# Kernel optimization log

Measured on AMD Instinct MI355X. Metric: run time of the kernel, lower is better.

Reference implementation:

```python
import jax, jax.numpy as jnp
import numpy as np

DIM = 2048
DIM_HEAD = 128
HEADS = 16
FF_MULT = 4
ATTN_INNER = DIM_HEAD * HEADS            # 2048
FF_INNER = DIM * FF_MULT                 # 8192
FUSED_OUT = ATTN_INNER + 2 * DIM_HEAD + 2 * FF_INNER  # 18688
EPS = 1e-5


def setup_inputs() -> dict:
    key = jax.random.key(0)
    ks = jax.random.split(key, 5)
    B, N = 1, 2048
    x = jax.random.normal(ks[0], (B, N, DIM), dtype=jnp.float32)
    gamma = jnp.ones((DIM,), dtype=jnp.float32)
    # store weights as [in, out] for x @ W
    w_fused = jax.random.normal(ks[1], (DIM, FUSED_OUT), dtype=jnp.float32) * (DIM ** -0.5)
    w_attn_out = jax.random.normal(ks[2], (ATTN_INNER, DIM), dtype=jnp.float32) * (ATTN_INNER ** -0.5)
    w_ff_out = jax.random.normal(ks[3], (FF_INNER, DIM), dtype=jnp.float32) * (FF_INNER ** -0.5)
    return {"x": x, "gamma": gamma, "w_fused": w_fused,
            "w_attn_out": w_attn_out, "w_ff_out": w_ff_out}


def reference(x, gamma, w_fused, w_attn_out, w_ff_out):
    b, n, d = x.shape
    h, dh = HEADS, DIM_HEAD
    scale = dh ** -0.5

    # LayerNorm (beta fixed at 0)
    mu = jnp.mean(x, axis=-1, keepdims=True)
    var = jnp.mean(jnp.square(x - mu), axis=-1, keepdims=True)
    xn = (x - mu) * jax.lax.rsqrt(var + EPS) * gamma

    # fused QKV + FF projection
    proj = xn @ w_fused  # [b, n, FUSED_OUT]
    q = proj[..., :ATTN_INNER]
    k = proj[..., ATTN_INNER:ATTN_INNER + dh]
    v = proj[..., ATTN_INNER + dh:ATTN_INNER + 2 * dh]
    ff = proj[..., ATTN_INNER + 2 * dh:]

    # multi-query attention: q per-head, k/v shared
    q = q.reshape(b, n, h, dh).transpose(0, 2, 1, 3) * scale  # [b,h,n,dh]
    sim = jnp.einsum('bhid,bjd->bhij', q, k)
    causal = jnp.triu(jnp.ones((n, n), dtype=bool), k=1)
    neg = -jnp.finfo(sim.dtype).max
    sim = jnp.where(causal, neg, sim)
    attn = jax.nn.softmax(sim, axis=-1)
    out = jnp.einsum('bhij,bjd->bhid', attn, v)
    out = out.transpose(0, 2, 1, 3).reshape(b, n, h * dh)
    attn_out = out @ w_attn_out

    # parallel SwiGLU FFN
    ff_x, gate = jnp.split(ff, 2, axis=-1)
    ff_out = (jax.nn.silu(gate) * ff_x) @ w_ff_out

    return attn_out + ff_out
```

## Files before the change

kernel.cpp:

```cpp
#include <hip/hip_runtime.h>
#include <hip/hip_bf16.h>

typedef unsigned short u16;
typedef __bf16 bf16x8 __attribute__((ext_vector_type(8)));
typedef float f32x4 __attribute__((ext_vector_type(4)));

#define DIM 2048
#define SEQ 2048
#define HEADS 16
#define DH 128
#define FUSED_OUT 18688
#define FF_INNER 8192
#define KOFF 2048
#define VOFF 2176
#define FFOFF 2304
#define AE_LD 10240

#define WS_XN   0
#define WS_WFT  8388608
#define WS_PROJ 84934656
#define WS_VT   161480704
#define WS_BTE  0
#define WS_AE   41943040

__device__ __forceinline__ float b2f(u16 u) {
  union { unsigned int i; float f; } c; c.i = ((unsigned int)u) << 16; return c.f;
}
__device__ __forceinline__ u16 f2b(float f) {
  union { float f; unsigned int i; } c; c.f = f;
  return (u16)((c.i + 0x7fffu + ((c.i >> 16) & 1u)) >> 16);
}
__device__ __forceinline__ void async16(void* lds, const void* g) {
  __builtin_amdgcn_global_load_lds((const __attribute__((address_space(1))) unsigned int*)g,
                                   (__attribute__((address_space(3))) unsigned int*)lds,
                                   16, 0, 0);
}

union U8 { uint4 v; u16 s[8]; };

__global__ void __launch_bounds__(256) ln_kernel(const float* __restrict__ x,
                                                 const float* __restrict__ gamma,
                                                 u16* __restrict__ xn) {
  const int row = blockIdx.x, tid = threadIdx.x;
  const int lane = tid & 63, wv = tid >> 6;
  float v[8], s1 = 0.f, s2 = 0.f;
  {
    float4 a0 = *(const float4*)(x + (size_t)row * DIM + tid * 8);
    float4 a1 = *(const float4*)(x + (size_t)row * DIM + tid * 8 + 4);
    v[0] = a0.x; v[1] = a0.y; v[2] = a0.z; v[3] = a0.w;
    v[4] = a1.x; v[5] = a1.y; v[6] = a1.z; v[7] = a1.w;
  }
#pragma unroll
  for (int i = 0; i < 8; ++i) { s1 += v[i]; s2 += v[i] * v[i]; }
#pragma unroll
  for (int off = 32; off > 0; off >>= 1) {
    s1 += __shfl_down(s1, off, 64);
    s2 += __shfl_down(s2, off, 64);
  }
  __shared__ float r1[4], r2[4];
  if (lane == 0) { r1[wv] = s1; r2[wv] = s2; }
  __syncthreads();
  s1 = r1[0] + r1[1] + r1[2] + r1[3];
  s2 = r2[0] + r2[1] + r2[2] + r2[3];
  const float inv = 1.0f / DIM;
  const float mu = s1 * inv;
  const float var = s2 * inv - mu * mu;
  const float rs = rsqrtf(var + 1e-5f);
  float4 g0 = *(const float4*)(gamma + tid * 8);
  float4 g1 = *(const float4*)(gamma + tid * 8 + 4);
  const float gm[8] = {g0.x, g0.y, g0.z, g0.w, g1.x, g1.y, g1.z, g1.w};
  U8 o;
#pragma unroll
  for (int i = 0; i < 8; ++i) o.s[i] = f2b((v[i] - mu) * rs * gm[i]);
  *(uint4*)(xn + (size_t)row * DIM + tid * 8) = o.v;
}

__global__ void __launch_bounds__(256) transpose_f2b64(const float* __restrict__ in,
                                                       u16* __restrict__ out,
                                                       int ldin, int ldout) {
  __shared__ u16 t[64][65];
  const int tx = threadIdx.x, ty = threadIdx.y;
  const int r0 = blockIdx.y * 64, c0 = blockIdx.x * 64;
#pragma unroll
  for (int i = 0; i < 16; ++i)
    t[ty + i * 4][tx] = f2b(in[(size_t)(r0 + ty + i * 4) * ldin + c0 + tx]);
  __syncthreads();
#pragma unroll
  for (int i = 0; i < 16; ++i)
    out[(size_t)(c0 + ty + i * 4) * ldout + r0 + tx] = t[tx][ty + i * 4];
}

__global__ void __launch_bounds__(256) trans_wout64(const float* __restrict__ w_attn,
                                                    const float* __restrict__ w_ff,
                                                    u16* __restrict__ BtE) {
  __shared__ u16 t[64][65];
  const int tx = threadIdx.x, ty = threadIdx.y;
  const int c0 = blockIdx.x * 64;
  const float* in; int r0, kout;
  if (blockIdx.y < 32) { in = w_attn; r0 = blockIdx.y * 64; kout = r0; }
  else { in = w_ff; r0 = (blockIdx.y - 32) * 64; kout = 2048 + r0; }
#pragma unroll
  for (int i = 0; i < 16; ++i)
    t[ty + i * 4][tx] = f2b(in[(size_t)(r0 + ty + i * 4) * DIM + c0 + tx]);
  __syncthreads();
#pragma unroll
  for (int i = 0; i < 16; ++i)
    BtE[(size_t)(c0 + ty + i * 4) * AE_LD + kout + tx] = t[tx][ty + i * 4];
}

__global__ void __launch_bounds__(256) transpose_u16_64(const u16* __restrict__ in,
                                                        u16* __restrict__ out,
                                                        int ldin, int ldout) {
  __shared__ u16 t[64][65];
  const int tx = threadIdx.x, ty = threadIdx.y;
  const int r0 = blockIdx.y * 64, c0 = blockIdx.x * 64;
#pragma unroll
  for (int i = 0; i < 16; ++i)
    t[ty + i * 4][tx] = in[(size_t)(r0 + ty + i * 4) * ldin + c0 + tx];
  __syncthreads();
#pragma unroll
  for (int i = 0; i < 16; ++i)
    out[(size_t)(c0 + ty + i * 4) * ldout + r0 + tx] = t[tx][ty + i * 4];
}

template <int OUTMODE>
__global__ void __launch_bounds__(256) gemm_bt(const u16* __restrict__ A,
                                               const u16* __restrict__ Bt,
                                               void* __restrict__ Cv,
                                               int Ksz, int lda, int ldb, int ldc) {
  __shared__ alignas(16) u16 sA[128 * 64];
  __shared__ alignas(16) u16 sB[128 * 64];
  const int tid = threadIdx.x;
  const int lane = tid & 63, wv = tid >> 6;
  const int lhalf = lane & 15, lgrp = lane >> 4;
  const int m0 = blockIdx.x * 128, n0 = blockIdx.y * 128;
  const int kbeg = blockIdx.z * Ksz, kend = kbeg + Ksz;
  const int wr = (wv >> 1) * 64, wc = (wv & 1) * 64;
  const f32x4 fzero = {0.f, 0.f, 0.f, 0.f};

  const int srow = lane >> 3;
  const int scol = ((lane & 7) ^ srow) * 8;
  const int key = lhalf & 7;

  f32x4 acc[4][4];
#pragma unroll
  for (int i = 0; i < 4; ++i)
#pragma unroll
    for (int j = 0; j < 4; ++j) acc[i][j] = fzero;

  for (int k0 = kbeg; k0 < kend; k0 += 64) {
#pragma unroll
    for (int c = 0; c < 4; ++c) {
      const int row = c * 32 + wv * 8 + srow;
      const int ldsoff = (c * 4096 + wv * 1024) >> 1;
      async16(&sA[ldsoff], A + (size_t)(m0 + row) * lda + k0 + scol);
      async16(&sB[ldsoff], Bt + (size_t)(n0 + row) * ldb + k0 + scol);
    }
    __syncthreads();
#pragma unroll
    for (int kk = 0; kk < 64; kk += 32) {
      bf16x8 af[4], bfr[4];
#pragma unroll
      for (int i = 0; i < 4; ++i)
        af[i] = *(const bf16x8*)&sA[(wr + i * 16 + lhalf) * 64 + ((((kk >> 3) + lgrp) ^ key) << 3)];
#pragma unroll
      for (int j = 0; j < 4; ++j)
        bfr[j] = *(const bf16x8*)&sB[(wc + j * 16 + lhalf) * 64 + ((((kk >> 3) + lgrp) ^ key) << 3)];
#pragma unroll
      for (int i = 0; i < 4; ++i)
#pragma unroll
        for (int j = 0; j < 4; ++j)
          acc[i][j] = __builtin_amdgcn_mfma_f32_16x16x32_bf16(af[i], bfr[j], acc[i][j], 0, 0, 0);
    }
    __syncthreads();
  }
#pragma unroll
  for (int i = 0; i < 4; ++i)
#pragma unroll
    for (int j = 0; j < 4; ++j)
#pragma unroll
      for (int t = 0; t < 4; ++t) {
        const int row = m0 + wr + i * 16 + lgrp * 4 + t;
        const int col = n0 + wc + j * 16 + lhalf;
        if (OUTMODE == 0) ((u16*)Cv)[(size_t)row * ldc + col] = f2b(acc[i][j][t]);
        else atomicAdd((float*)Cv + (size_t)row * ldc + col, acc[i][j][t]);
      }
}

__global__ void __launch_bounds__(256) attn_kernel(const u16* __restrict__ proj,
                                                   const u16* __restrict__ Vt,
                                                   u16* __restrict__ Ae) {
  const int h = blockIdx.y, qi = blockIdx.x;
  const int tid = threadIdx.x;
  const int lane = tid & 63, wv = tid >> 6;
  const int lhalf = lane & 15, lgrp = lane >> 4;
  const int key = lhalf & 7;

  __shared__ alignas(16) u16 Ks[128 * 128];
  __shared__ alignas(16) u16 Vts[128 * 128];
  __shared__ alignas(16) u16 Ps[4][16 * 128];

  const int sr = lane >> 4;
  const int sb = lane & 15;

  bf16x8 aq[4];
  {
    const u16* gq = proj + (size_t)(qi * 64 + wv * 16 + lhalf) * FUSED_OUT + h * DH;
#pragma unroll
    for (int kk = 0; kk < 4; ++kk) aq[kk] = *(const bf16x8*)(gq + kk * 32 + lgrp * 8);
  }
  const f32x4 fzero = {0.f, 0.f, 0.f, 0.f};
  f32x4 o[8];
#pragma unroll
  for (int i = 0; i < 8; ++i) o[i] = fzero;
  float mrow[4] = {-__builtin_inff(), -__builtin_inff(), -__builtin_inff(), -__builtin_inff()};
  float lrow[4] = {0.f, 0.f, 0.f, 0.f};
  const float scale = 0.088388347648318447f;
  const int jmax = (qi * 64 + 63) >> 7;

  for (int jt = 0; jt <= jmax; ++jt) {
    __syncthreads();
#pragma unroll
    for (int i = 0; i < 8; ++i) {
      const int ch = wv * 8 + i;
      const int row = ch * 4 + sr;
      const int gb = sb ^ (row & 7);
      async16(&Ks[ch * 512], proj + (size_t)(jt * 128 + row) * FUSED_OUT + KOFF + gb * 8);
      async16(&Vts[ch * 512], Vt + (size_t)row * SEQ + jt * 128 + gb * 8);
    }
    __syncthreads();
    f32x4 s[8];
#pragma unroll
    for (int sub = 0; sub < 8; ++sub) {
      f32x4 a = fzero;
#pragma unroll
      for (int kk = 0; kk < 4; ++kk) {
        bf16x8 bk = *(const bf16x8*)&Ks[(sub * 16 + lhalf) * 128 + (((kk * 4 + lgrp) ^ key) << 3)];
        a = __builtin_amdgcn_mfma_f32_16x16x32_bf16(aq[kk], bk, a, 0, 0, 0);
      }
      s[sub] = a;
    }
    const int row_g = qi * 64 + wv * 16 + lgrp * 4;
    const int col_b = jt * 128 + lhalf;
#pragma unroll
    for (int t = 0; t < 4; ++t) {
      float mx = -__builtin_inff();
#pragma unroll
      for (int sub = 0; sub < 8; ++sub) {
        float v = s[sub][t] * scale;
        if (col_b + sub * 16 > row_g + t) v = -__builtin_inff();
        s[sub][t] = v;
        mx = fmaxf(mx, v);
      }
      mx = fmaxf(mx, __shfl_xor(mx, 1, 64));
      mx = fmaxf(mx, __shfl_xor(mx, 2, 64));
      mx = fmaxf(mx, __shfl_xor(mx, 4, 64));
      mx = fmaxf(mx, __shfl_xor(mx, 8, 64));
      const float mnew = fmaxf(mrow[t], mx);
      const float alpha = __expf(mrow[t] - mnew);
      mrow[t] = mnew;
      float ls = 0.f;
#pragma unroll
      for (int sub = 0; sub < 8; ++sub) {
        const float p = __expf(s[sub][t] - mnew);
        s[sub][t] = p;
        ls += p;
      }
      ls += __shfl_xor(ls, 1, 64);
      ls += __shfl_xor(ls, 2, 64);
      ls += __shfl_xor(ls, 4, 64);
      ls += __shfl_xor(ls, 8, 64);
      lrow[t] = lrow[t] * alpha + ls;
      const int prow = lgrp * 4 + t;
      const int pkey = prow & 7;
#pragma unroll
      for (int sub = 0; sub < 8; ++sub) {
        o[sub][t] *= alpha;
        const int b = sub * 2 + (lhalf >> 3);
        Ps[wv][prow * 128 + ((b ^ pkey) << 3) + (lhalf & 7)] = f2b(s[sub][t]);
      }
    }
    asm volatile("s_waitcnt lgkmcnt(0)" ::: "memory");
#pragma unroll
    for (int kk = 0; kk < 4; ++kk) {
      bf16x8 ap = *(const bf16x8*)&Ps[wv][lhalf * 128 + (((kk * 4 + lgrp) ^ key) << 3)];
#pragma unroll
      for (int sub = 0; sub < 8; ++sub) {
        bf16x8 bv = *(const bf16x8*)&Vts[(sub * 16 + lhalf) * 128 + (((kk * 4 + lgrp) ^ key) << 3)];
        o[sub] = __builtin_amdgcn_mfma_f32_16x16x32_bf16(ap, bv, o[sub], 0, 0, 0);
      }
    }
  }
#pragma unroll
  for (int sub = 0; sub < 8; ++sub)
#pragma unroll
    for (int t = 0; t < 4; ++t) {
      const int row = qi * 64 + wv * 16 + lgrp * 4 + t;
      const int col = h * DH + sub * 16 + lhalf;
      Ae[(size_t)row * AE_LD + col] = f2b(o[sub][t] / lrow[t]);
    }
}

__global__ void __launch_bounds__(256) ffa_kernel(const u16* __restrict__ proj,
                                                  u16* __restrict__ Ae) {
  const size_t idx = (size_t)blockIdx.x * 256 + threadIdx.x;
  const size_t e = idx * 8;
  const int row = (int)(e >> 13);
  const int j = (int)(e & 8191);
  const u16* base = proj + (size_t)row * FUSED_OUT + FFOFF;
  U8 xr, gr, os;
  xr.v = *(const uint4*)(base + j);
  gr.v = *(const uint4*)(base + FF_INNER + j);
#pragma unroll
  for (int i = 0; i < 8; ++i) {
    const float g = b2f(gr.s[i]);
    const float sg = g / (1.f + __expf(-g));
    os.s[i] = f2b(sg * b2f(xr.s[i]));
  }
  *(uint4*)(Ae + (size_t)row * AE_LD + 2048 + j) = os.v;
}

extern "C" void kernel_launch(void* const* d_in, const int* in_sizes, int n_in,
                              void* d_out, int out_size, void* d_ws, size_t ws_size,
                              hipStream_t stream) {
  const float* x       = (const float*)d_in[0];
  const float* gamma   = (const float*)d_in[1];
  const float* w_fused = (const float*)d_in[2];
  const float* w_attn  = (const float*)d_in[3];
  const float* w_ff    = (const float*)d_in[4];
  float* out = (float*)d_out;
  char* ws = (char*)d_ws;
  u16* xn   = (u16*)(ws + WS_XN);
  u16* wfT  = (u16*)(ws + WS_WFT);
  u16* proj = (u16*)(ws + WS_PROJ);
  u16* Vt   = (u16*)(ws + WS_VT);
  u16* BtE  = (u16*)(ws + WS_BTE);
  u16* Ae   = (u16*)(ws + WS_AE);

  hipMemsetAsync(d_out, 0, (size_t)out_size * sizeof(float), stream);

  ln_kernel<<<dim3(2048), dim3(256), 0, stream>>>(x, gamma, xn);
  transpose_f2b64<<<dim3(292, 32), dim3(64, 4), 0, stream>>>(w_fused, wfT, FUSED_OUT, DIM);
  gemm_bt<0><<<dim3(16, 146, 1), dim3(256), 0, stream>>>(xn, wfT, proj, DIM, DIM, DIM, FUSED_OUT);

  transpose_u16_64<<<dim3(2, 32), dim3(64, 4), 0, stream>>>(proj + VOFF, Vt, FUSED_OUT, SEQ);
  trans_wout64<<<dim3(32, 160), dim3(64, 4), 0, stream>>>(w_attn, w_ff, BtE);
  attn_kernel<<<dim3(32, 16), dim3(256), 0, stream>>>(proj, Vt, Ae);
  ffa_kernel<<<dim3(8192), dim3(256), 0, stream>>>(proj, Ae);

  gemm_bt<2><<<dim3(16, 16, 2), dim3(256), 0, stream>>>(Ae, BtE, out, AE_LD / 2, AE_LD, AE_LD, DIM);
}
```

Baseline: 720.8 us.

## Replace GEMM with 256x256 tiled, 8-wave, double-buffered, ping-pong pipelined kernel

Replaces the 128x128 single-buffered GEMM with a 256x256 tile kernel using 512 threads (8 waves) and double-buffered LDS. Global-to-LDS loads for the next K-step are issued in quarters between MFMA groups, using explicit waitcnt, barriers and setprio so loads overlap with compute. The output GEMM now uses a split-K of 4 instead of 2. The goal is higher MFMA utilization and more reuse per tile, at the cost of heavy LDS use (128KB), more registers, fewer blocks, and more atomic traffic from the larger split-K.

```diff
diff --git a/kernel.cpp b/kernel.cpp
--- a/kernel.cpp
+++ b/kernel.cpp
@@ -123,67 +123,128 @@
     out[(size_t)(c0 + ty + i * 4) * ldout + r0 + tx] = t[tx][ty + i * 4];
 }
 
+#define BAR()    asm volatile("s_barrier" ::: "memory")
+#define LGKM0()  asm volatile("s_waitcnt lgkmcnt(0)" ::: "memory")
+#define RA(mi, kk) (*(const bf16x8*)&sA[c][(wm * 128 + (mi) * 16 + lhalf) * 64 + ((((kk) * 4 + lgrp) ^ key) << 3)])
+#define RB(ni, kk) (*(const bf16x8*)&sB[c][(wn * 64 + (ni) * 16 + lhalf) * 64 + ((((kk) * 4 + lgrp) ^ key) << 3)])
+#define MFMA_Q(MB, AA)                                                   \
+  _Pragma("unroll") for (int kk = 0; kk < 2; ++kk)                       \
+  _Pragma("unroll") for (int u = 0; u < 2; ++u)                          \
+  _Pragma("unroll") for (int ni = 0; ni < 4; ++ni)                       \
+      acc[(MB) + u][ni] = __builtin_amdgcn_mfma_f32_16x16x32_bf16(       \
+          AA[u][kk], bF[ni][kk], acc[(MB) + u][ni], 0, 0, 0);
+
+__device__ __forceinline__ void stage_h(u16* lds, const u16* g, int ld,
+                                        int wv, int srow, int scol) {
+  async16(lds + wv * 512,        g + (size_t)(wv * 8 + srow) * ld + scol);
+  async16(lds + 4096 + wv * 512, g + (size_t)(64 + wv * 8 + srow) * ld + scol);
+}
+
 template <int OUTMODE>
-__global__ void __launch_bounds__(256) gemm_bt(const u16* __restrict__ A,
-                                               const u16* __restrict__ Bt,
-                                               void* __restrict__ Cv,
-                                               int Ksz, int lda, int ldb, int ldc) {
-  __shared__ alignas(16) u16 sA[128 * 64];
-  __shared__ alignas(16) u16 sB[128 * 64];
+__global__ void __launch_bounds__(512, 2) gemm8p(const u16* __restrict__ A,
+                                                 const u16* __restrict__ Bt,
+                                                 void* __restrict__ Cv,
+                                                 int Ksz, int lda, int ldb, int ldc) {
+  __shared__ alignas(16) u16 sA[2][256 * 64];
+  __shared__ alignas(16) u16 sB[2][256 * 64];
   const int tid = threadIdx.x;
   const int lane = tid & 63, wv = tid >> 6;
+  const int wm = wv >> 2, wn = wv & 3;
   const int lhalf = lane & 15, lgrp = lane >> 4;
-  const int m0 = blockIdx.x * 128, n0 = blockIdx.y * 128;
-  const int kbeg = blockIdx.z * Ksz, kend = kbeg + Ksz;
-  const int wr = (wv >> 1) * 64, wc = (wv & 1) * 64;
+  const int key = lhalf & 7;
+  const int srow = lane >> 3;
+  const int scol = ((lane & 7) ^ srow) << 3;
+  const int m0 = blockIdx.x * 256, n0 = blockIdx.y * 256;
+  const int kbeg = blockIdx.z * Ksz;
+  const int NT = Ksz >> 6;
+
+  const u16* Abase = A + (size_t)m0 * lda + kbeg;
+  const u16* Bbase = Bt + (size_t)n0 * ldb + kbeg;
+
+  stage_h(&sB[0][0],    Bbase,                     ldb, wv, srow, scol);
+  stage_h(&sB[0][8192], Bbase + (size_t)128 * ldb, ldb, wv, srow, scol);
+  stage_h(&sA[0][0],    Abase,                     lda, wv, srow, scol);
+  stage_h(&sA[0][8192], Abase + (size_t)128 * lda, lda, wv, srow, scol);
+  asm volatile("s_waitcnt vmcnt(4)" ::: "memory");
+  stage_h(&sB[1][0],    Bbase + 64,                     ldb, wv, srow, scol);
+  stage_h(&sB[1][8192], Bbase + (size_t)128 * ldb + 64, ldb, wv, srow, scol);
+  stage_h(&sA[1][0],    Abase + 64,                     lda, wv, srow, scol);
+  asm volatile("s_waitcnt vmcnt(6)" ::: "memory");
+  BAR();
+
+  f32x4 acc[8][4];
   const f32x4 fzero = {0.f, 0.f, 0.f, 0.f};
-
-  const int srow = lane >> 3;
-  const int scol = ((lane & 7) ^ srow) * 8;
-  const int key = lhalf & 7;
-
-  f32x4 acc[4][4];
-#pragma unroll
-  for (int i = 0; i < 4; ++i)
+#pragma unroll
+  for (int i = 0; i < 8; ++i)
 #pragma unroll
     for (int j = 0; j < 4; ++j) acc[i][j] = fzero;
 
-  for (int k0 = kbeg; k0 < kend; k0 += 64) {
-#pragma unroll
-    for (int c = 0; c < 4; ++c) {
-      const int row = c * 32 + wv * 8 + srow;
-      const int ldsoff = (c * 4096 + wv * 1024) >> 1;
-      async16(&sA[ldsoff], A + (size_t)(m0 + row) * lda + k0 + scol);
-      async16(&sB[ldsoff], Bt + (size_t)(n0 + row) * ldb + k0 + scol);
-    }
-    __syncthreads();
-#pragma unroll
-    for (int kk = 0; kk < 64; kk += 32) {
-      bf16x8 af[4], bfr[4];
-#pragma unroll
-      for (int i = 0; i < 4; ++i)
-        af[i] = *(const bf16x8*)&sA[(wr + i * 16 + lhalf) * 64 + ((((kk >> 3) + lgrp) ^ key) << 3)];
-#pragma unroll
-      for (int j = 0; j < 4; ++j)
-        bfr[j] = *(const bf16x8*)&sB[(wc + j * 16 + lhalf) * 64 + ((((kk >> 3) + lgrp) ^ key) << 3)];
-#pragma unroll
-      for (int i = 0; i < 4; ++i)
-#pragma unroll
-        for (int j = 0; j < 4; ++j)
-          acc[i][j] = __builtin_amdgcn_mfma_f32_16x16x32_bf16(af[i], bfr[j], acc[i][j], 0, 0, 0);
-    }
-    __syncthreads();
-  }
-#pragma unroll
-  for (int i = 0; i < 4; ++i)
-#pragma unroll
-    for (int j = 0; j < 4; ++j)
-#pragma unroll
-      for (int t = 0; t < 4; ++t) {
-        const int row = m0 + wr + i * 16 + lgrp * 4 + t;
-        const int col = n0 + wc + j * 16 + lhalf;
-        if (OUTMODE == 0) ((u16*)Cv)[(size_t)row * ldc + col] = f2b(acc[i][j][t]);
-        else atomicAdd((float*)Cv + (size_t)row * ldc + col, acc[i][j][t]);
+  bf16x8 bF[4][2];
+  bf16x8 aF[2][2];
+  bf16x8 aX[2][2];
+
+  int t1w = 1;
+  int t2w = 2 % NT;
+  for (int t = 0; t < NT; ++t) {
+    const int c = t & 1;
+#pragma unroll
+    for (int kk = 0; kk < 2; ++kk) {
+      aF[0][kk] = RA(0, kk); aF[1][kk] = RA(1, kk);
+#pragma unroll
+      for (int ni = 0; ni < 4; ++ni) bF[ni][kk] = RB(ni, kk);
+    }
+    stage_h(&sA[c ^ 1][8192], Abase + (size_t)128 * lda + t1w * 64, lda, wv, srow, scol);
+    asm volatile("s_waitcnt lgkmcnt(8)" ::: "memory");
+    BAR(); LGKM0();
+    __builtin_amdgcn_s_setprio(1);
+    MFMA_Q(0, aF);
+    __builtin_amdgcn_s_setprio(0);
+    BAR();
+#pragma unroll
+    for (int kk = 0; kk < 2; ++kk) { aF[0][kk] = RA(2, kk); aF[1][kk] = RA(3, kk); }
+    stage_h(&sB[c][0], Bbase + t2w * 64, ldb, wv, srow, scol);
+    BAR(); LGKM0();
+    __builtin_amdgcn_s_setprio(1);
+    MFMA_Q(2, aF);
+    __builtin_amdgcn_s_setprio(0);
+    BAR();
+#pragma unroll
+    for (int kk = 0; kk < 2; ++kk) { aF[0][kk] = RA(4, kk); aF[1][kk] = RA(5, kk); }
+    if (wm == 0) {
+#pragma unroll
+      for (int kk = 0; kk < 2; ++kk) { aX[0][kk] = RA(6, kk); aX[1][kk] = RA(7, kk); }
+    }
+    stage_h(&sB[c][8192], Bbase + (size_t)128 * ldb + t2w * 64, ldb, wv, srow, scol);
+    BAR(); LGKM0();
+    __builtin_amdgcn_s_setprio(1);
+    MFMA_Q(4, aF);
+    __builtin_amdgcn_s_setprio(0);
+    BAR();
+    if (wm != 0) {
+#pragma unroll
+      for (int kk = 0; kk < 2; ++kk) { aF[0][kk] = RA(6, kk); aF[1][kk] = RA(7, kk); }
+    }
+    stage_h(&sA[c][0], Abase + t2w * 64, lda, wv, srow, scol);
+    asm volatile("s_waitcnt vmcnt(6)" ::: "memory");
+    BAR(); LGKM0();
+    __builtin_amdgcn_s_setprio(1);
+    if (wm == 0) { MFMA_Q(6, aX); } else { MFMA_Q(6, aF); }
+    __builtin_amdgcn_s_setprio(0);
+    BAR();
+    t1w = (t1w + 1 == NT) ? 0 : t1w + 1;
+    t2w = (t2w + 1 == NT) ? 0 : t2w + 1;
+  }
+  asm volatile("s_waitcnt vmcnt(0)" ::: "memory");
+#pragma unroll
+  for (int mi = 0; mi < 8; ++mi)
+#pragma unroll
+    for (int ni = 0; ni < 4; ++ni)
+#pragma unroll
+      for (int tt = 0; tt < 4; ++tt) {
+        const int row = m0 + wm * 128 + mi * 16 + lgrp * 4 + tt;
+        const int col = n0 + wn * 64 + ni * 16 + lhalf;
+        if (OUTMODE == 0) ((u16*)Cv)[(size_t)row * ldc + col] = f2b(acc[mi][ni][tt]);
+        else atomicAdd((float*)Cv + (size_t)row * ldc + col, acc[mi][ni][tt]);
       }
 }
 
@@ -341,12 +402,12 @@
 
   ln_kernel<<<dim3(2048), dim3(256), 0, stream>>>(x, gamma, xn);
   transpose_f2b64<<<dim3(292, 32), dim3(64, 4), 0, stream>>>(w_fused, wfT, FUSED_OUT, DIM);
-  gemm_bt<0><<<dim3(16, 146, 1), dim3(256), 0, stream>>>(xn, wfT, proj, DIM, DIM, DIM, FUSED_OUT);
+  gemm8p<0><<<dim3(8, 73, 1), dim3(512), 0, stream>>>(xn, wfT, proj, DIM, DIM, DIM, FUSED_OUT);
 
   transpose_u16_64<<<dim3(2, 32), dim3(64, 4), 0, stream>>>(proj + VOFF, Vt, FUSED_OUT, SEQ);
   trans_wout64<<<dim3(32, 160), dim3(64, 4), 0, stream>>>(w_attn, w_ff, BtE);
   attn_kernel<<<dim3(32, 16), dim3(256), 0, stream>>>(proj, Vt, Ae);
   ffa_kernel<<<dim3(8192), dim3(256), 0, stream>>>(proj, Ae);
 
-  gemm_bt<2><<<dim3(16, 16, 2), dim3(256), 0, stream>>>(Ae, BtE, out, AE_LD / 2, AE_LD, AE_LD, DIM);
-}
+  gemm8p<2><<<dim3(8, 8, 4), dim3(512), 0, stream>>>(Ae, BtE, out, AE_LD / 4, AE_LD, AE_LD, DIM);
+}
```

Result: slower. 745.1 us (+3.4%).
